# Optimization experiments

Measured on AMD Instinct MI355X. Metric: run time of the kernel, lower is better.

The kernel has to match this reference:

```python
import jax, jax.numpy as jnp
import numpy as np

LN_EPS = 1e-5
LOCAL_SIZE = 256
N_HEAD, D_HEAD = 16, 64


def layer_norm_c(x):
    # layer norm over channel dim (axis=1), no affine params (matches F.layer_norm(x.T,(d,)).T)
    m = jnp.mean(x, axis=1, keepdims=True)
    v = jnp.var(x, axis=1, keepdims=True)
    return (x - m) / jnp.sqrt(v + LN_EPS)


def rel_shift(x):
    # x: [b, n, q, k] -> Transformer-XL relative shift
    b, n, q, k = x.shape
    x = jnp.pad(x, ((0, 0), (0, 0), (0, 0), (1, 0)))
    return x.reshape(b, n, k + 1, q)[:, :, 1:].reshape(b, n, q, k)


def setup_inputs() -> dict:
    key = jax.random.key(0)
    ks = jax.random.split(key, 14)
    bsz, d_model, qlen, mlen = 4, 1024, 512, 512
    klen = qlen + mlen
    d_inner = 4096
    s = lambda k, shape, sc=0.05: jax.random.normal(k, shape, dtype=jnp.float32) * sc
    return {
        "z1ss": jax.random.normal(ks[0], (bsz, d_model, qlen), dtype=jnp.float32),
        "uss": jax.random.normal(ks[1], (bsz, 3 * d_model, klen), dtype=jnp.float32) * 0.1,
        "z0": jax.random.normal(ks[2], (bsz, d_model, mlen), dtype=jnp.float32),
        "pos_emb": jax.random.normal(ks[3], (1, d_model, klen), dtype=jnp.float32),
        "qkv_w": s(ks[4], (3 * d_model, d_model)),
        "r_w": s(ks[5], (d_model, d_model)),
        "r_w_bias": s(ks[6], (N_HEAD, D_HEAD)),
        "r_r_bias": s(ks[7], (N_HEAD, D_HEAD)),
        "o_w": s(ks[8], (d_model, d_model)),
        "o_b": s(ks[9], (d_model,)),
        "ff1_w": s(ks[10], (d_inner, d_model)),
        "ff1_b": s(ks[11], (d_inner,)),
        "ff2_w": s(ks[12], (d_model, d_inner)),
        "ff2_b": s(ks[13], (d_model,)),
    }


def reference(z1ss, uss, z0, pos_emb, qkv_w, r_w, r_w_bias, r_r_bias, o_w, o_b,
              ff1_w, ff1_b, ff2_w, ff2_b):
    bsz, d_model, qlen = z1ss.shape
    mlen = z0.shape[2]
    n_head, d_head = N_HEAD, D_HEAD
    scale = 1.0 / d_head ** 0.5

    # ---- self-attention (post-lnorm path) ----
    cat = jnp.concatenate([z0, z1ss], axis=-1)              # [b, d, klen]
    klen = cat.shape[2]
    w_heads = jnp.einsum('od,bdk->bok', qkv_w, cat) + uss   # [b, 3d, klen]
    r_head_k = jnp.einsum('od,dk->ok', r_w, pos_emb[0])     # [d, rlen]
    rlen = r_head_k.shape[1]

    w_head_q, w_head_k, w_head_v = jnp.split(w_heads, 3, axis=1)
    w_head_q = w_head_q[:, :, -qlen:]
    w_head_q = w_head_q.reshape(bsz, n_head, d_head, qlen)
    w_head_k = w_head_k.reshape(bsz, n_head, d_head, klen)
    w_head_v = w_head_v.reshape(bsz, n_head, d_head, klen)
    r_head_k = r_head_k.reshape(n_head, d_head, rlen)

    rw_q = w_head_q + r_w_bias[:, :, None]                  # [b,n,d,q]
    AC = jnp.einsum('bndi,bndj->bnij', rw_q, w_head_k)      # [b,n,q,k]
    rr_q = w_head_q + r_r_bias[:, :, None]
    BD = rel_shift(jnp.einsum('bndi,ndj->bnij', rr_q, r_head_k))
    attn_score = (AC + BD) * scale

    local_size = LOCAL_SIZE if LOCAL_SIZE else 1000
    i = jnp.arange(qlen)[:, None]
    j = jnp.arange(klen)[None, :]
    mask = (j > i + mlen) | (j <= i + mlen - local_size)    # causal + local window
    attn_score = jnp.where(mask[None, None], -jnp.inf, attn_score)

    attn_prob = jax.nn.softmax(attn_score, axis=-1)
    attn_vec = jnp.einsum('bnij,bndj->bndi', attn_prob, w_head_v)
    attn_vec = attn_vec.reshape(bsz, n_head * d_head, qlen)
    attn_out = jnp.einsum('od,bdq->boq', o_w, attn_vec) + o_b[None, :, None]
    x = layer_norm_c(attn_out + z1ss)                       # post-lnorm

    # ---- position-wise FF (weight-shared, post-lnorm) ----
    h = jax.nn.relu(jnp.einsum('id,bdq->biq', ff1_w, x) + ff1_b[None, :, None])
    out2 = jnp.einsum('di,biq->bdq', ff2_w, h) + ff2_b[None, :, None]
    return layer_norm_c(out2 + x)
```

## Files before the change

### kernel.cpp

```cpp
#include <hip/hip_runtime.h>
#include <hip/hip_bf16.h>

typedef unsigned short u16;
typedef __attribute__((ext_vector_type(8))) short s8v;
typedef __attribute__((ext_vector_type(4))) short s4v;
typedef __attribute__((ext_vector_type(4))) float f4v;

__device__ __forceinline__ float s2f(u16 s) {
    unsigned int u = ((unsigned int)s) << 16;
    return __builtin_bit_cast(float, u);
}
__device__ __forceinline__ u16 f2s(float f) {
    __hip_bfloat16 h = __float2bfloat16(f);
    return __builtin_bit_cast(u16, h);
}

__device__ __forceinline__ void gl2lds16(const u16* g, u16* l) {
    __builtin_amdgcn_global_load_lds((const __attribute__((address_space(1))) void*)g,
                                     (__attribute__((address_space(3))) void*)l, 16, 0, 0);
}

#define BSZ 4
#define DM 1024
#define QLEN 512
#define MLEN 512
#define KLEN 1024
#define DI 4096
#define NH 16
#define DH 64
#define WIN 256

#define CONV_BLKS 13312
#define Z0_BLKS 2048
#define Z1_BLKS 2048
#define POS_BLKS 256
__global__ __launch_bounds__(256) void prep(
    const float* __restrict__ qkv_w, const float* __restrict__ r_w,
    const float* __restrict__ o_w, const float* __restrict__ ff1_w,
    const float* __restrict__ ff2_w,
    u16* __restrict__ wQ, u16* __restrict__ wR, u16* __restrict__ wO,
    u16* __restrict__ wF1, u16* __restrict__ wF2,
    const float* __restrict__ z0, const float* __restrict__ z1ss,
    const float* __restrict__ pos,
    u16* __restrict__ catT, u16* __restrict__ posT)
{
    int bx = blockIdx.x, tid = threadIdx.x;
    if (bx < CONV_BLKS) {
        const int e0 = 786432, e1 = e0 + 262144, e2 = e1 + 262144, e3 = e2 + 1048576;
        int i = bx * 256 + tid;
        const float* s; u16* d; int off;
        if (i < e0)      { s = qkv_w; d = wQ;  off = i; }
        else if (i < e1) { s = r_w;   d = wR;  off = i - e0; }
        else if (i < e2) { s = o_w;   d = wO;  off = i - e1; }
        else if (i < e3) { s = ff1_w; d = wF1; off = i - e2; }
        else             { s = ff2_w; d = wF2; off = i - e3; }
        f4v v = *(const f4v*)&s[(size_t)off * 4];
        s4v o;
#pragma unroll
        for (int k = 0; k < 4; ++k) o[k] = (short)f2s(v[k]);
        *(s4v*)&d[(size_t)off * 4] = o;
        return;
    }
    __shared__ float tile[32][33];
    int tx = tid & 31, ty = tid >> 5;
    const float* src; u16* dst; long sS, sD; int ldS, ldD, colOff, rowOff, t0, f0, b;
    if (bx < CONV_BLKS + Z0_BLKS) {
        int idx = bx - CONV_BLKS;
        t0 = (idx & 15) * 32; f0 = ((idx >> 4) & 31) * 32; b = idx >> 9;
        src = z0;   sS = (long)DM * MLEN; ldS = MLEN; colOff = 0;
        dst = catT; sD = (long)KLEN * DM; ldD = DM;  rowOff = 0;
    } else if (bx < CONV_BLKS + Z0_BLKS + Z1_BLKS) {
        int idx = bx - CONV_BLKS - Z0_BLKS;
        t0 = (idx & 15) * 32; f0 = ((idx >> 4) & 31) * 32; b = idx >> 9;
        src = z1ss; sS = (long)DM * QLEN; ldS = QLEN; colOff = 0;
        dst = catT; sD = (long)KLEN * DM; ldD = DM;  rowOff = MLEN;
    } else {
        int idx = bx - CONV_BLKS - Z0_BLKS - Z1_BLKS;
        t0 = (idx & 7) * 32; f0 = (idx >> 3) * 32; b = 0;
        src = pos;  sS = 0; ldS = KLEN; colOff = KLEN - WIN;
        dst = posT; sD = 0; ldD = DM;   rowOff = 0;
    }
#pragma unroll
    for (int p = 0; p < 4; ++p)
        tile[ty + 8 * p][tx] = src[(size_t)b * sS + (size_t)(f0 + ty + 8 * p) * ldS + colOff + t0 + tx];
    __syncthreads();
#pragma unroll
    for (int p = 0; p < 4; ++p)
        dst[(size_t)b * sD + (size_t)(rowOff + t0 + ty + 8 * p) * ldD + f0 + tx] = f2s(tile[tx][ty + 8 * p]);
}

__global__ __launch_bounds__(256) void uss_add(
    const float* __restrict__ uss, u16* __restrict__ whT, u16* __restrict__ vT)
{
    __shared__ float tile[32][33];
    int b = blockIdx.z;
    int t0 = blockIdx.x * 32, fy = blockIdx.y;
    int tx = threadIdx.x, ty = threadIdx.y;
    if (fy < 32 && t0 < 512) return;
    const float* S = uss + (size_t)b * 3072 * 1024;
    if (fy < 64) {
        int f0 = fy * 32;
        u16* D = whT + (size_t)b * 1024 * 3072;
#pragma unroll
        for (int p = 0; p < 4; ++p)
            tile[ty + 8 * p][tx] = S[(size_t)(f0 + ty + 8 * p) * 1024 + t0 + tx];
        __syncthreads();
#pragma unroll
        for (int p = 0; p < 4; ++p) {
            size_t o = (size_t)(t0 + ty + 8 * p) * 3072 + f0 + tx;
            D[o] = f2s(s2f(D[o]) + tile[tx][ty + 8 * p]);
        }
    } else {
        int d0 = (fy - 64) * 32;
#pragma unroll
        for (int p = 0; p < 4; ++p) {
            int d = d0 + ty + 8 * p;
            size_t ui = ((size_t)2048 + d) * 1024 + t0 + tx;
            size_t vi = (size_t)d * 4096 + (size_t)b * KLEN + t0 + tx;
            vT[vi] = f2s(s2f(vT[vi]) + S[ui]);
        }
    }
}

template<int BN, int SPLIT>
__global__ __launch_bounds__(256) void gemm_bt(
    const u16* __restrict__ A,
    const u16* __restrict__ B,
    u16* __restrict__ C,
    float* __restrict__ fOut,
    int M, int K,
    const float* __restrict__ bias,
    int relu,
    int qskip,
    long pstride,
    u16* __restrict__ vTout,
    const u16* __restrict__ A2,
    const u16* __restrict__ B2,
    u16* __restrict__ C2,
    float* __restrict__ fOut2,
    long pstride2)
{
    constexpr int BM = 128, BK = 64;
    constexpr int MI = (BN == 128) ? 4 : 2;
    constexpr int NI = 4;
    int n0, m0, Mv;
    const u16* Ap; const u16* Bp; u16* Cp;
    bool isR = false;
    if (A2 && blockIdx.y == gridDim.y - 1) {
        if (blockIdx.x >= 32) return;
        isR = true;
        n0 = (blockIdx.x & 3) * BN;
        m0 = (blockIdx.x >> 2) * BM;
        Ap = A2; Bp = B2; Cp = C2; Mv = 1024;
    } else {
        n0 = blockIdx.x * BN; m0 = blockIdx.y * BM;
        if (qskip && m0 + BM <= 1024 && (n0 & 1023) < 512) return;
        Ap = A; Bp = B; Cp = C; Mv = M;
    }
    const int Ks = K / SPLIT;
    const int kbeg = blockIdx.z * Ks;
    __shared__ __align__(16) u16 As[BM * BK];
    __shared__ __align__(16) u16 Bs[BN * BK];
    const int tid = threadIdx.x, lane = tid & 63, wv = tid >> 6;
    const int l15 = lane & 15, quad = lane >> 4;
    const int wm = (BN == 128) ? (wv >> 1) * 64 : wv * 32;
    const int wn = (BN == 128) ? (wv & 1) * 64 : 0;
    f4v acc[MI][NI] = {};
    for (int kk = kbeg; kk < kbeg + Ks; kk += BK) {
        __syncthreads();
#pragma unroll
        for (int p = 0; p < (BM * 8) / 256; ++p) {
            int c = p * 256 + tid, r = c >> 3, q = c & 7, qs = q ^ (r & 7);
            gl2lds16(&Ap[(size_t)(m0 + r) * K + kk + qs * 8], &As[c * 8]);
        }
#pragma unroll
        for (int p = 0; p < (BN * 8) / 256; ++p) {
            int c = p * 256 + tid, r = c >> 3, q = c & 7, qs = q ^ (r & 7);
            gl2lds16(&Bp[(size_t)(n0 + r) * K + kk + qs * 8], &Bs[c * 8]);
        }
        __syncthreads();
#pragma unroll
        for (int k0 = 0; k0 < BK; k0 += 32) {
            s8v af[MI], bf[NI];
#pragma unroll
            for (int mi = 0; mi < MI; ++mi) {
                int r = wm + mi * 16 + l15;
                af[mi] = *(const s8v*)&As[r * BK + ((((k0 >> 3) + quad) ^ (r & 7)) << 3)];
            }
#pragma unroll
            for (int ni = 0; ni < NI; ++ni) {
                int r = wn + ni * 16 + l15;
                bf[ni] = *(const s8v*)&Bs[r * BK + ((((k0 >> 3) + quad) ^ (r & 7)) << 3)];
            }
#pragma unroll
            for (int mi = 0; mi < MI; ++mi)
#pragma unroll
                for (int ni = 0; ni < NI; ++ni)
                    acc[mi][ni] = __builtin_amdgcn_mfma_f32_16x16x32_bf16(af[mi], bf[ni], acc[mi][ni], 0, 0, 0);
        }
    }
    if (SPLIT > 1) {
        int z = blockIdx.z;
        float* base = (z < 2) ? fOut + (long)z * pstride
                              : fOut2 + (long)(z - 2) * pstride2;
#pragma unroll
        for (int mi = 0; mi < MI; ++mi) {
            int m = m0 + wm + mi * 16 + quad * 4;
#pragma unroll
            for (int ni = 0; ni < NI; ++ni) {
                int n = n0 + wn + ni * 16 + l15;
                *(f4v*)&base[(size_t)n * Mv + m] = acc[mi][ni];
            }
        }
    } else if (vTout && !isR && m0 >= 2048) {
#pragma unroll
        for (int mi = 0; mi < MI; ++mi) {
            int m = m0 + wm + mi * 16 + quad * 4;
#pragma unroll
            for (int ni = 0; ni < NI; ++ni) {
                int n = n0 + wn + ni * 16 + l15;
#pragma unroll
                for (int r2 = 0; r2 < 4; ++r2)
                    vTout[(size_t)(m + r2 - 2048) * 4096 + n] = f2s(acc[mi][ni][r2]);
            }
        }
    } else {
#pragma unroll
        for (int mi = 0; mi < MI; ++mi) {
            int m = m0 + wm + mi * 16 + quad * 4;
            float bv[4] = {0.f, 0.f, 0.f, 0.f};
            if (bias && !isR) {
#pragma unroll
                for (int r2 = 0; r2 < 4; ++r2) bv[r2] = bias[m + r2];
            }
#pragma unroll
            for (int ni = 0; ni < NI; ++ni) {
                int n = n0 + wn + ni * 16 + l15;
                float o[4];
#pragma unroll
                for (int r2 = 0; r2 < 4; ++r2) o[r2] = acc[mi][ni][r2] + bv[r2];
                if (relu && !isR) {
#pragma unroll
                    for (int r2 = 0; r2 < 4; ++r2) o[r2] = fmaxf(o[r2], 0.f);
                }
                s4v st;
#pragma unroll
                for (int r2 = 0; r2 < 4; ++r2) st[r2] = (short)f2s(o[r2]);
                *(s4v*)&Cp[(size_t)n * Mv + m] = st;
            }
        }
    }
}

#define QT 64
#define SROW 260
__global__ __launch_bounds__(256, 2) void attn_mfma(
    const u16* __restrict__ WHT,
    const u16* __restrict__ VT,
    const u16* __restrict__ RT,
    const float* __restrict__ rwb, const float* __restrict__ rrb,
    u16* __restrict__ avT)
{
    __shared__ __align__(16) float sS[QT * SROW];

    const int qt = blockIdx.x, n = blockIdx.y, b = blockIdx.z;
    const int i0 = qt * QT, j0 = i0 + WIN + 1;
    const int tid = threadIdx.x, lane = tid & 63, wv = tid >> 6;
    const int l15 = lane & 15, quad = lane >> 4;
    const u16* W = WHT + (size_t)b * KLEN * (3 * DM);

    s8v qac[4][2], qbd[4][2];
#pragma unroll
    for (int h = 0; h < 4; ++h) {
        int qrow = MLEN + i0 + 16 * h + l15;
#pragma unroll
        for (int kc = 0; kc < 2; ++kc) {
            int col = n * DH + kc * 32 + quad * 8;
            s8v qv = *(const s8v*)&W[(size_t)qrow * (3 * DM) + col];
            s8v a, c;
#pragma unroll
            for (int e = 0; e < 8; ++e) {
                float qf = s2f((u16)qv[e]);
                a[e] = (short)f2s(qf + rwb[col + e]);
                c[e] = (short)f2s(qf + rrb[col + e]);
            }
            qac[h][kc] = a; qbd[h][kc] = c;
        }
    }

    for (int ci = wv; ci < 20; ci += 4) {
        int j = j0 + ci * 16 + l15; if (j > KLEN - 1) j = KLEN - 1;
        const u16* Kr = &W[(size_t)j * (3 * DM) + DM + n * DH + quad * 8];
        s8v k0 = *(const s8v*)Kr, k1 = *(const s8v*)(Kr + 32);
#pragma unroll
        for (int h = 0; h < 4; ++h) {
            f4v acc = {};
            acc = __builtin_amdgcn_mfma_f32_16x16x32_bf16(qac[h][0], k0, acc, 0, 0, 0);
            acc = __builtin_amdgcn_mfma_f32_16x16x32_bf16(qac[h][1], k1, acc, 0, 0, 0);
#pragma unroll
            for (int r2 = 0; r2 < 4; ++r2) {
                int qi = 16 * h + quad * 4 + r2;
                int t = ci * 16 + l15 - qi;
                if ((unsigned)t < 256u) sS[qi * SROW + t] = acc[r2];
            }
        }
    }
    __syncthreads();

#pragma unroll
    for (int cc = 0; cc < 4; ++cc) {
        int ci = wv + cc * 4;
        const u16* Rr = &RT[(size_t)(ci * 16 + l15) * DM + n * DH + quad * 8];
        s8v r0 = *(const s8v*)Rr, r1 = *(const s8v*)(Rr + 32);
#pragma unroll
        for (int h = 0; h < 4; ++h) {
            f4v acc = {};
            acc = __builtin_amdgcn_mfma_f32_16x16x32_bf16(qbd[h][0], r0, acc, 0, 0, 0);
            acc = __builtin_amdgcn_mfma_f32_16x16x32_bf16(qbd[h][1], r1, acc, 0, 0, 0);
#pragma unroll
            for (int r2 = 0; r2 < 4; ++r2) {
                int qi = 16 * h + quad * 4 + r2;
                sS[qi * SROW + ci * 16 + l15] += acc[r2];
            }
        }
    }
    __syncthreads();

    {
        int g = tid >> 4, l = tid & 15;
#pragma unroll
        for (int h = 0; h < 4; ++h) {
            int r = g + 16 * h;
            float vals[16], mx = -1e30f;
#pragma unroll
            for (int k = 0; k < 16; ++k) {
                float s = sS[r * SROW + l + 16 * k] * 0.125f;
                vals[k] = s; mx = fmaxf(mx, s);
            }
            asm volatile("" ::: "memory");
#pragma unroll
            for (int d = 1; d < 16; d <<= 1) mx = fmaxf(mx, __shfl_xor(mx, d, 16));
            float sum = 0.f;
#pragma unroll
            for (int k = 0; k < 16; ++k) { vals[k] = __expf(vals[k] - mx); sum += vals[k]; }
#pragma unroll
            for (int d = 1; d < 16; d <<= 1) sum += __shfl_xor(sum, d, 16);
            float inv = 1.f / sum;
            u16* sPr = (u16*)&sS[r * SROW];
#pragma unroll
            for (int k = 0; k < 16; ++k) sPr[r + 1 + l + 16 * k] = f2s(vals[k] * inv);
            for (int p = l; p <= r; p += 16) sPr[p] = 0;
            for (int p = r + 257 + l; p < 320; p += 16) sPr[p] = 0;
        }
    }
    __syncthreads();

    const u16* sPu = (const u16*)sS;
    const size_t vbase = (size_t)(n * DH + wv * 16 + l15) * 4096
                       + (size_t)b * KLEN + (j0 - 1) + quad * 8;
    f4v o[4] = {};
#pragma unroll
    for (int kc = 0; kc < 10; ++kc) {
        s8v bb = *(const s8v*)&VT[vbase + kc * 32];
#pragma unroll
        for (int h = 0; h < 4; ++h) {
            s8v a = *(const s8v*)&sPu[(size_t)(16 * h + l15) * (2 * SROW) + kc * 32 + quad * 8];
            o[h] = __builtin_amdgcn_mfma_f32_16x16x32_bf16(a, bb, o[h], 0, 0, 0);
        }
    }
#pragma unroll
    for (int h = 0; h < 4; ++h)
#pragma unroll
        for (int r2 = 0; r2 < 4; ++r2) {
            int qi = quad * 4 + r2;
            avT[((size_t)b * QLEN + i0 + 16 * h + qi) * DM + n * DH + wv * 16 + l15] = f2s(o[h][r2]);
        }
}

__global__ __launch_bounds__(256) void ln_f(
    const float* __restrict__ P, long pstride, int nparts,
    const float* __restrict__ bias,
    const u16* __restrict__ res, int resMode, u16* __restrict__ out)
{
    int n = blockIdx.x, tid = threadIdx.x;
    int lane = tid & 63, wv = tid >> 6;
    int f = tid * 4;
    int rrow = resMode ? (((n >> 9) * 2 + 1) * 512 + (n & 511)) : n;
    f4v pv = *(const f4v*)&P[(size_t)n * DM + f];
    for (int p = 1; p < nparts; ++p) {
        const float* Pp = P + (long)p * pstride;
        pv += *(const f4v*)&Pp[(size_t)n * DM + f];
    }
    s4v rv = *(const s4v*)&res[(size_t)rrow * DM + f];
    f4v bv = *(const f4v*)&bias[f];
    float v[4];
#pragma unroll
    for (int k = 0; k < 4; ++k) v[k] = pv[k] + bv[k] + s2f((u16)rv[k]);
    float s = v[0] + v[1] + v[2] + v[3];
    float ss = v[0] * v[0] + v[1] * v[1] + v[2] * v[2] + v[3] * v[3];
#pragma unroll
    for (int d = 1; d < 64; d <<= 1) {
        s += __shfl_xor(s, d, 64);
        ss += __shfl_xor(ss, d, 64);
    }
    __shared__ float ps[4], pss[4];
    if (lane == 0) { ps[wv] = s; pss[wv] = ss; }
    __syncthreads();
    float S = ps[0] + ps[1] + ps[2] + ps[3];
    float SS = pss[0] + pss[1] + pss[2] + pss[3];
    float m = S * (1.f / DM);
    float var = SS * (1.f / DM) - m * m;
    float inv = rsqrtf(fmaxf(var, 0.f) + 1e-5f);
    s4v st;
#pragma unroll
    for (int k = 0; k < 4; ++k) st[k] = (short)f2s((v[k] - m) * inv);
    *(s4v*)&out[(size_t)n * DM + f] = st;
}

#define LNR 16
#define LROW 1030
__global__ __launch_bounds__(256) void ln_out(
    const float* __restrict__ P0, const float* __restrict__ P1,
    const float* __restrict__ P2, const float* __restrict__ P3,
    const float* __restrict__ bias, const u16* __restrict__ res,
    float* __restrict__ out)
{
    __shared__ float rows[LNR * LROW];
    __shared__ float sm[LNR], si[LNR];
    int n0 = blockIdx.x * LNR;
    int tid = threadIdx.x;
    int r = tid >> 4, l = tid & 15;
    int n = n0 + r;
    float s = 0.f, ss = 0.f;
    for (int k = 0; k < 16; ++k) {
        int f = (l + 16 * k) * 4;
        f4v v = *(const f4v*)&P0[(size_t)n * DM + f];
        v += *(const f4v*)&P1[(size_t)n * DM + f];
        v += *(const f4v*)&P2[(size_t)n * DM + f];
        v += *(const f4v*)&P3[(size_t)n * DM + f];
        s4v rv = *(const s4v*)&res[(size_t)n * DM + f];
        f4v bv = *(const f4v*)&bias[f];
        float* dst = &rows[r * LROW + f];
#pragma unroll
        for (int j = 0; j < 4; ++j) {
            float x = v[j] + bv[j] + s2f((u16)rv[j]);
            dst[j] = x;
            s += x; ss += x * x;
        }
    }
#pragma unroll
    for (int d = 1; d < 16; d <<= 1) {
        s += __shfl_xor(s, d, 16);
        ss += __shfl_xor(ss, d, 16);
    }
    if (l == 0) {
        float m = s * (1.f / DM);
        float var = ss * (1.f / DM) - m * m;
        sm[r] = m; si[r] = rsqrtf(fmaxf(var, 0.f) + 1e-5f);
    }
    __syncthreads();
    int b = n0 >> 9, q0 = n0 & 511;
    int qi = tid & 15, g = tid >> 4;
    float m = sm[qi], inv = si[qi];
    float* O = out + (size_t)b * DM * QLEN + q0 + qi;
    for (int k = 0; k < 64; ++k) {
        int f = g + 16 * k;
        O[(size_t)f * QLEN] = (rows[qi * LROW + f] - m) * inv;
    }
}

extern "C" void kernel_launch(void* const* d_in, const int* in_sizes, int n_in,
                              void* d_out, int out_size, void* d_ws, size_t ws_size,
                              hipStream_t stream) {
    const float* z1ss  = (const float*)d_in[0];
    const float* uss   = (const float*)d_in[1];
    const float* z0    = (const float*)d_in[2];
    const float* pos   = (const float*)d_in[3];
    const float* qkv_w = (const float*)d_in[4];
    const float* r_w   = (const float*)d_in[5];
    const float* rwb   = (const float*)d_in[6];
    const float* rrb   = (const float*)d_in[7];
    const float* o_w   = (const float*)d_in[8];
    const float* o_b   = (const float*)d_in[9];
    const float* ff1_w = (const float*)d_in[10];
    const float* ff1_b = (const float*)d_in[11];
    const float* ff2_w = (const float*)d_in[12];
    const float* ff2_b = (const float*)d_in[13];

    u16* ws = (u16*)d_ws;
    u16* wQ   = ws;
    u16* wR   = ws + 3145728;
    u16* wO   = ws + 4194304;
    u16* wF1  = ws + 5242880;
    u16* wF2  = ws + 9437184;
    u16* catT = ws + 13631488;
    u16* whT  = ws + 17825792;
    u16* posT = ws + 30408704;
    u16* rT   = ws + 30670848;
    u16* avT  = ws + 30932992;
    u16* xT   = ws + 33030144;
    float* pref = (float*)(ws + 35127296);
    u16* hT   = whT;

    u16* vT = (u16*)pref;

    float* part1 = (float*)d_ws;
    float* part2 = (float*)(ws + 4194304);
    float* part3 = (float*)catT;
    long pstr  = part1 - pref;
    long pstr2 = part3 - part2;

    dim3 tblk(32, 8);

    prep<<<CONV_BLKS + Z0_BLKS + Z1_BLKS + POS_BLKS, 256, 0, stream>>>(
        qkv_w, r_w, o_w, ff1_w, ff2_w, wQ, wR, wO, wF1, wF2,
        z0, z1ss, pos, catT, posT);

    gemm_bt<64, 1><<<dim3(64, 25, 1), 256, 0, stream>>>(
        wQ, catT, whT, nullptr, 3 * DM, DM, nullptr, 0, 1, 0, vT,
        wR, posT, rT, nullptr, 0);

    uss_add<<<dim3(32, 96, BSZ), tblk, 0, stream>>>(uss, whT, vT);

    attn_mfma<<<dim3(QLEN / QT, NH, BSZ), 256, 0, stream>>>(whT, vT, rT, rwb, rrb, avT);

    gemm_bt<64, 2><<<dim3(32, 8, 2), 256, 0, stream>>>(
        wO, avT, nullptr, pref, DM, DM, nullptr, 0, 0, pstr, nullptr,
        nullptr, nullptr, nullptr, nullptr, 0);

    ln_f<<<2048, 256, 0, stream>>>(pref, pstr, 2, o_b, catT, 1, xT);

    gemm_bt<64, 1><<<dim3(32, 32, 1), 256, 0, stream>>>(
        wF1, xT, hT, nullptr, DI, DM, ff1_b, 1, 0, 0, nullptr,
        nullptr, nullptr, nullptr, nullptr, 0);

    gemm_bt<64, 4><<<dim3(32, 8, 4), 256, 0, stream>>>(
        wF2, hT, nullptr, pref, DM, DI, nullptr, 0, 0, pstr, nullptr,
        nullptr, nullptr, nullptr, part2, pstr2);

    ln_out<<<2048 / LNR, 256, 0, stream>>>(
        pref, part1, part2, part3, ff2_b, xT, (float*)d_out);
}
```

Baseline: 318.5 us.

## Fuse uss addition into QKV GEMM epilogue and run R-projection in skipped blocks

```diff
diff --git a/kernel.cpp b/kernel.cpp
--- a/kernel.cpp
+++ b/kernel.cpp
@@ -89,39 +89,6 @@
         dst[(size_t)b * sD + (size_t)(rowOff + t0 + ty + 8 * p) * ldD + f0 + tx] = f2s(tile[tx][ty + 8 * p]);
 }
 
-__global__ __launch_bounds__(256) void uss_add(
-    const float* __restrict__ uss, u16* __restrict__ whT, u16* __restrict__ vT)
-{
-    __shared__ float tile[32][33];
-    int b = blockIdx.z;
-    int t0 = blockIdx.x * 32, fy = blockIdx.y;
-    int tx = threadIdx.x, ty = threadIdx.y;
-    if (fy < 32 && t0 < 512) return;
-    const float* S = uss + (size_t)b * 3072 * 1024;
-    if (fy < 64) {
-        int f0 = fy * 32;
-        u16* D = whT + (size_t)b * 1024 * 3072;
-#pragma unroll
-        for (int p = 0; p < 4; ++p)
-            tile[ty + 8 * p][tx] = S[(size_t)(f0 + ty + 8 * p) * 1024 + t0 + tx];
-        __syncthreads();
-#pragma unroll
-        for (int p = 0; p < 4; ++p) {
-            size_t o = (size_t)(t0 + ty + 8 * p) * 3072 + f0 + tx;
-            D[o] = f2s(s2f(D[o]) + tile[tx][ty + 8 * p]);
-        }
-    } else {
-        int d0 = (fy - 64) * 32;
-#pragma unroll
-        for (int p = 0; p < 4; ++p) {
-            int d = d0 + ty + 8 * p;
-            size_t ui = ((size_t)2048 + d) * 1024 + t0 + tx;
-            size_t vi = (size_t)d * 4096 + (size_t)b * KLEN + t0 + tx;
-            vT[vi] = f2s(s2f(vT[vi]) + S[ui]);
-        }
-    }
-}
-
 template<int BN, int SPLIT>
 __global__ __launch_bounds__(256) void gemm_bt(
     const u16* __restrict__ A,
@@ -133,6 +100,7 @@
     int relu,
     int qskip,
     long pstride,
+    const float* __restrict__ uss,
     u16* __restrict__ vTout,
     const u16* __restrict__ A2,
     const u16* __restrict__ B2,
@@ -143,19 +111,17 @@
     constexpr int BM = 128, BK = 64;
     constexpr int MI = (BN == 128) ? 4 : 2;
     constexpr int NI = 4;
-    int n0, m0, Mv;
-    const u16* Ap; const u16* Bp; u16* Cp;
+    int n0 = blockIdx.x * BN, m0 = blockIdx.y * BM, Mv = M;
+    const u16* Ap = A; const u16* Bp = B; u16* Cp = C;
     bool isR = false;
-    if (A2 && blockIdx.y == gridDim.y - 1) {
-        if (blockIdx.x >= 32) return;
-        isR = true;
-        n0 = (blockIdx.x & 3) * BN;
-        m0 = (blockIdx.x >> 2) * BM;
-        Ap = A2; Bp = B2; Cp = C2; Mv = 1024;
-    } else {
-        n0 = blockIdx.x * BN; m0 = blockIdx.y * BM;
-        if (qskip && m0 + BM <= 1024 && (n0 & 1023) < 512) return;
-        Ap = A; Bp = B; Cp = C; Mv = M;
+    if (qskip && m0 + BM <= 1024 && (n0 & 1023) < 512) {
+        if (A2 && blockIdx.y == 0) {
+            int rid = (blockIdx.x & 7) | ((blockIdx.x >> 4) << 3);
+            isR = true;
+            n0 = (rid & 3) * BN;
+            m0 = (rid >> 2) * BM;
+            Ap = A2; Bp = B2; Cp = C2; Mv = 1024;
+        } else return;
     }
     const int Ks = K / SPLIT;
     const int kbeg = blockIdx.z * Ks;
@@ -219,9 +185,12 @@
 #pragma unroll
             for (int ni = 0; ni < NI; ++ni) {
                 int n = n0 + wn + ni * 16 + l15;
-#pragma unroll
-                for (int r2 = 0; r2 < 4; ++r2)
-                    vTout[(size_t)(m + r2 - 2048) * 4096 + n] = f2s(acc[mi][ni][r2]);
+                int b = n >> 10, t = n & 1023;
+#pragma unroll
+                for (int r2 = 0; r2 < 4; ++r2) {
+                    float u = uss[((size_t)b * 3072 + m + r2) * 1024 + t];
+                    vTout[(size_t)(m + r2 - 2048) * 4096 + n] = f2s(acc[mi][ni][r2] + u);
+                }
             }
         }
     } else {
@@ -239,6 +208,12 @@
                 float o[4];
 #pragma unroll
                 for (int r2 = 0; r2 < 4; ++r2) o[r2] = acc[mi][ni][r2] + bv[r2];
+                if (uss && !isR) {
+                    int b = n >> 10, t = n & 1023;
+#pragma unroll
+                    for (int r2 = 0; r2 < 4; ++r2)
+                        o[r2] += uss[((size_t)b * 3072 + m + r2) * 1024 + t];
+                }
                 if (relu && !isR) {
 #pragma unroll
                     for (int r2 = 0; r2 < 4; ++r2) o[r2] = fmaxf(o[r2], 0.f);
@@ -510,32 +485,28 @@
     long pstr  = part1 - pref;
     long pstr2 = part3 - part2;
 
-    dim3 tblk(32, 8);
-
     prep<<<CONV_BLKS + Z0_BLKS + Z1_BLKS + POS_BLKS, 256, 0, stream>>>(
         qkv_w, r_w, o_w, ff1_w, ff2_w, wQ, wR, wO, wF1, wF2,
         z0, z1ss, pos, catT, posT);
 
-    gemm_bt<64, 1><<<dim3(64, 25, 1), 256, 0, stream>>>(
-        wQ, catT, whT, nullptr, 3 * DM, DM, nullptr, 0, 1, 0, vT,
+    gemm_bt<64, 1><<<dim3(64, 24, 1), 256, 0, stream>>>(
+        wQ, catT, whT, nullptr, 3 * DM, DM, nullptr, 0, 1, 0, uss, vT,
         wR, posT, rT, nullptr, 0);
 
-    uss_add<<<dim3(32, 96, BSZ), tblk, 0, stream>>>(uss, whT, vT);
-
     attn_mfma<<<dim3(QLEN / QT, NH, BSZ), 256, 0, stream>>>(whT, vT, rT, rwb, rrb, avT);
 
     gemm_bt<64, 2><<<dim3(32, 8, 2), 256, 0, stream>>>(
-        wO, avT, nullptr, pref, DM, DM, nullptr, 0, 0, pstr, nullptr,
+        wO, avT, nullptr, pref, DM, DM, nullptr, 0, 0, pstr, nullptr, nullptr,
         nullptr, nullptr, nullptr, nullptr, 0);
 
     ln_f<<<2048, 256, 0, stream>>>(pref, pstr, 2, o_b, catT, 1, xT);
 
     gemm_bt<64, 1><<<dim3(32, 32, 1), 256, 0, stream>>>(
-        wF1, xT, hT, nullptr, DI, DM, ff1_b, 1, 0, 0, nullptr,
+        wF1, xT, hT, nullptr, DI, DM, ff1_b, 1, 0, 0, nullptr, nullptr,
         nullptr, nullptr, nullptr, nullptr, 0);
 
     gemm_bt<64, 4><<<dim3(32, 8, 4), 256, 0, stream>>>(
-        wF2, hT, nullptr, pref, DM, DI, nullptr, 0, 0, pstr, nullptr,
+        wF2, hT, nullptr, pref, DM, DI, nullptr, 0, 0, pstr, nullptr, nullptr,
         nullptr, nullptr, nullptr, part2, pstr2);
 
     ln_out<<<2048 / LNR, 256, 0, stream>>>(
```

Result: faster. 304.2 us (-4.5%).
